# Optimization experiments

Measured on AMD Instinct MI355X. Metric: run time of the kernel, lower is better.

## Reference

```python
import jax, jax.numpy as jnp
import numpy as np

V, E, H, B, TS, TT = 32000, 256, 512, 32, 512, 128


def setup_inputs() -> dict:
    key = jax.random.key(0)
    ks = jax.random.split(key, 20)
    s_e = 1.0 / np.sqrt(E)
    s_h = 1.0 / np.sqrt(H)
    n = jax.random.normal
    return {
        "src": jax.random.randint(ks[0], (B, TS), 0, V),
        "tgt": jax.random.randint(ks[1], (B, TT), 0, V),
        "tf_mask": jax.random.randint(ks[2], (TT - 1,), 0, 2),
        "emb_enc": n(ks[3], (V, E), jnp.float32) * 0.02,
        "emb_dec": n(ks[4], (V, E), jnp.float32) * 0.02,
        "enc_Wih0": n(ks[5], (E, H), jnp.float32) * s_e,
        "enc_Whh0": n(ks[6], (H, H), jnp.float32) * s_h,
        "enc_b0": jnp.zeros((H,), jnp.float32),
        "enc_Wih1": n(ks[7], (H, H), jnp.float32) * s_h,
        "enc_Whh1": n(ks[8], (H, H), jnp.float32) * s_h,
        "enc_b1": jnp.zeros((H,), jnp.float32),
        "dec_Wih0": n(ks[9], (E, H), jnp.float32) * s_e,
        "dec_Whh0": n(ks[10], (H, H), jnp.float32) * s_h,
        "dec_b0": jnp.zeros((H,), jnp.float32),
        "dec_Wih1": n(ks[11], (H, H), jnp.float32) * s_h,
        "dec_Whh1": n(ks[12], (H, H), jnp.float32) * s_h,
        "dec_b1": jnp.zeros((H,), jnp.float32),
        "dec_Wout": n(ks[13], (H, V), jnp.float32) * s_h,
        "dec_bout": jnp.zeros((V,), jnp.float32),
    }


def _cell(x, h, Wih0, Whh0, b0, Wih1, Whh1, b1):
    # x: (B, in), h: (2, B, H) -> new h (2, B, H). Vanilla tanh RNN, 2 layers.
    h0 = jnp.tanh(x @ Wih0 + h[0] @ Whh0 + b0)
    h1 = jnp.tanh(h0 @ Wih1 + h[1] @ Whh1 + b1)
    return jnp.stack([h0, h1])


def reference(src, tgt, tf_mask, emb_enc, emb_dec,
              enc_Wih0, enc_Whh0, enc_b0, enc_Wih1, enc_Whh1, enc_b1,
              dec_Wih0, dec_Whh0, dec_b0, dec_Wih1, dec_Whh1, dec_b1,
              dec_Wout, dec_bout):
    # ---- Encoder: run over TS steps, keep only final hidden (outputs unused by Seq2Seq) ----
    emb = emb_enc[src]                      # (B, TS, E)
    xs = jnp.swapaxes(emb, 0, 1)            # (TS, B, E)
    h0 = jnp.zeros((2, B, H), emb.dtype)

    def enc_step(h, x):
        return _cell(x, h, enc_Wih0, enc_Whh0, enc_b0, enc_Wih1, enc_Whh1, enc_b1), None

    enc_hidden, _ = jax.lax.scan(enc_step, h0, xs)

    def dec_step(carry, inp):
        h, tok = carry
        tgt_t, tf = inp
        x = emb_dec[tok]                    # (B, E)
        h_new = _cell(x, h, dec_Wih0, dec_Whh0, dec_b0, dec_Wih1, dec_Whh1, dec_b1)
        logits = h_new[1] @ dec_Wout + dec_bout   # (B, V)
        greedy = jnp.argmax(logits, axis=1).astype(tok.dtype)
        next_tok = jnp.where(tf > 0, tgt_t, greedy)
        return (h_new, next_tok), logits

    tgt_steps = jnp.swapaxes(tgt[:, 1:], 0, 1)   # (TT-1, B)
    (_, _), logits_seq = jax.lax.scan(dec_step, (enc_hidden, tgt[:, 0]), (tgt_steps, tf_mask))
    return jnp.swapaxes(logits_seq, 0, 1)        # (B, TT-1, V)
```

## Files before the change

kernel.cpp:

```cpp
#include <hip/hip_runtime.h>

#define V  32000
#define E  256
#define H  512
#define BB 32
#define TS 512
#define TT 128
#define NT 127

#define OFF_WBF  0ull
#define OFF_WT   8192000ull
#define OFF_PT   24576000ull
#define OFF_H0   24608000ull
#define OFF_H1   24640768ull
#define OFF_TOK  24673536ull
#define OFF_CNT  24673568ull

__device__ inline unsigned short f2bf(float f){
  unsigned int x = __float_as_uint(f);
  unsigned int r = x + 0x7fffu + ((x >> 16) & 1u);
  return (unsigned short)(r >> 16);
}
__device__ inline float bf2f(unsigned short u){
  return __uint_as_float(((unsigned int)u) << 16);
}

__device__ inline void top2_merge(float& v1,int& i1,float& v2,int& i2,
                                  float o1,int oi1,float o2,int oi2){
  if (o1 > v1 || (o1 == v1 && oi1 < i1)) {
    float nv2; int ni2;
    if (v1 > o2 || (v1 == o2 && i1 < oi2)) { nv2 = v1; ni2 = i1; }
    else { nv2 = o2; ni2 = oi2; }
    v1 = o1; i1 = oi1; v2 = nv2; i2 = ni2;
  } else if (o1 > v2 || (o1 == v2 && oi1 < i2)) {
    v2 = o1; i2 = oi1;
  }
}

__global__ void k_init(float* ws, const int* tgt){
  int gid = blockIdx.x*256 + threadIdx.x;
  float* h0 = ws + OFF_H0; float* h1 = ws + OFF_H1;
  if (gid < 2*BB*H){ h0[gid] = 0.f; h1[gid] = 0.f; }
  if (gid < BB) ((int*)(ws+OFF_TOK))[gid] = tgt[gid*TT + 0];
  if (gid == 0) ((int*)(ws+OFF_CNT))[0] = 0;
}

__global__ void k_wprep(float* ws, const float* wout){
  int tw = blockIdx.x; int k0 = (tw / 500) * 64; int v0 = (tw % 500) * 64;
  __shared__ float tile[64][65];
  unsigned short* wbf = (unsigned short*)(ws + OFF_WBF);
  float* wt = ws + OFF_WT;
  for (int i = threadIdx.x; i < 64*64; i += 256){
    int kk = i >> 6, vv = i & 63;
    float val = wout[(size_t)(k0+kk)*V + v0 + vv];
    tile[kk][vv] = val;
    wbf[(size_t)(k0+kk)*V + v0 + vv] = f2bf(val);
  }
  __syncthreads();
  for (int i = threadIdx.x; i < 64*64; i += 256){
    int vv = i >> 6, kk = i & 63;
    wt[(size_t)(v0+vv)*H + k0 + kk] = tile[kk][vv];
  }
}

__global__ void k_pre0(float* pre0, const int* src, const float* emb,
                       const float* Wih0, const float* b0){
  int t = blockIdx.x >> 2; int cb = blockIdx.x & 3;
  __shared__ int sidx[32];
  __shared__ float sA[32][257];
  int tid = threadIdx.x;
  if (tid < 32) sidx[tid] = src[tid*TS + t];
  __syncthreads();
  for (int i = tid; i < 32*E; i += 256){
    int bb = i >> 8, e = i & 255;
    sA[bb][e] = emb[(size_t)sidx[bb]*E + e];
  }
  __syncthreads();
  int c = tid & 127, rh = tid >> 7;
  int j = cb*128 + c;
  float bj = b0[j];
  float acc[16];
  #pragma unroll
  for (int i=0;i<16;i++) acc[i] = bj;
  for (int k=0;k<E;k++){
    float w = Wih0[(size_t)k*H + j];
    #pragma unroll
    for (int i=0;i<16;i++) acc[i] += sA[rh*16+i][k]*w;
  }
  #pragma unroll
  for (int i=0;i<16;i++){
    int b = rh*16 + i;
    pre0[((size_t)t*BB + b)*H + j] = acc[i];
  }
}

__global__ void k_enc(float* ws, const float* pre0, const float* Whh0,
                      const float* Wih1, const float* Whh1, const float* b1, int tau){
  float* h0 = ws + OFF_H0; float* h1 = ws + OFF_H1;
  int wg = blockIdx.x; int tid = threadIdx.x;
  if (wg < 64){
    if (tau >= TS) return;
    int rb = wg >> 3, cb = wg & 7;
    __shared__ float sh[4][513];
    const float* hprev = h0 + ((tau+1)&1)*BB*H;
    for (int i=tid;i<4*H;i+=256){ int rr=i>>9, k=i&511; sh[rr][k]=hprev[(rb*4+rr)*H+k]; }
    __syncthreads();
    int c = tid & 63, rsub = tid >> 6;
    int r = rb*4 + rsub, j = cb*64 + c;
    const float* w = Whh0 + j;
    float a0=0,a1=0,a2=0,a3=0;
    for (int k=0;k<H;k+=4){
      a0 += sh[rsub][k+0]*w[(size_t)(k+0)*H];
      a1 += sh[rsub][k+1]*w[(size_t)(k+1)*H];
      a2 += sh[rsub][k+2]*w[(size_t)(k+2)*H];
      a3 += sh[rsub][k+3]*w[(size_t)(k+3)*H];
    }
    float acc = pre0[((size_t)tau*BB + r)*H + j] + ((a0+a1)+(a2+a3));
    h0[(tau&1)*BB*H + r*H + j] = tanhf(acc);
  } else {
    if (tau < 1) return;
    int w2 = wg - 64;
    int rb = w2 >> 4, cb = w2 & 15;
    __shared__ float s0[4][513];
    __shared__ float s1[4][513];
    __shared__ float sp[256];
    const float* h0t = h0 + ((tau+1)&1)*BB*H;
    const float* h1p = h1 + (tau&1)*BB*H;
    for (int i=tid;i<4*H;i+=256){
      int rr=i>>9, k=i&511;
      s0[rr][k] = h0t[(rb*4+rr)*H+k];
      s1[rr][k] = h1p[(rb*4+rr)*H+k];
    }
    __syncthreads();
    int kh = tid >> 7, q = tid & 127;
    int c = q & 31, rsub = q >> 5;
    int r = rb*4 + rsub, j = cb*32 + c;
    const float* W = kh ? (Whh1 + j) : (Wih1 + j);
    float (*sh)[513] = kh ? s1 : s0;
    float a0=0,a1=0,a2=0,a3=0;
    for (int k=0;k<H;k+=4){
      a0 += sh[rsub][k+0]*W[(size_t)(k+0)*H];
      a1 += sh[rsub][k+1]*W[(size_t)(k+1)*H];
      a2 += sh[rsub][k+2]*W[(size_t)(k+2)*H];
      a3 += sh[rsub][k+3]*W[(size_t)(k+3)*H];
    }
    sp[tid] = ((a0+a1)+(a2+a3));
    __syncthreads();
    if (kh == 0){
      float v = sp[q] + sp[128+q] + b1[j];
      h1[((tau+1)&1)*BB*H + r*H + j] = tanhf(v);
    }
  }
}

__global__ void k_cellA(float* ws, const float* embd, const float* Wih0,
                        const float* Whh0, const float* b0, int t){
  float* h0 = ws + OFF_H0;
  const int* tok = (const int*)(ws + OFF_TOK);
  int rb = blockIdx.x >> 3, cb = blockIdx.x & 7;
  __shared__ int stok[4];
  __shared__ float sx[4][257];
  __shared__ float sh[4][513];
  int tid = threadIdx.x;
  if (tid < 4) stok[tid] = tok[rb*4 + tid];
  __syncthreads();
  for (int i=tid;i<4*E;i+=256){ int rr=i>>8, e=i&255; sx[rr][e] = embd[(size_t)stok[rr]*E + e]; }
  const float* hprev = h0 + ((t+1)&1)*BB*H;
  for (int i=tid;i<4*H;i+=256){ int rr=i>>9, k=i&511; sh[rr][k] = hprev[(rb*4+rr)*H + k]; }
  __syncthreads();
  int c = tid & 63, rsub = tid >> 6;
  int r = rb*4 + rsub, j = cb*64 + c;
  float a0=0,a1=0,a2=0,a3=0;
  for (int k=0;k<E;k+=4){
    a0 += sx[rsub][k+0]*Wih0[(size_t)(k+0)*H + j];
    a1 += sx[rsub][k+1]*Wih0[(size_t)(k+1)*H + j];
    a2 += sx[rsub][k+2]*Wih0[(size_t)(k+2)*H + j];
    a3 += sx[rsub][k+3]*Wih0[(size_t)(k+3)*H + j];
  }
  for (int k=0;k<H;k+=4){
    a0 += sh[rsub][k+0]*Whh0[(size_t)(k+0)*H + j];
    a1 += sh[rsub][k+1]*Whh0[(size_t)(k+1)*H + j];
    a2 += sh[rsub][k+2]*Whh0[(size_t)(k+2)*H + j];
    a3 += sh[rsub][k+3]*Whh0[(size_t)(k+3)*H + j];
  }
  h0[(t&1)*BB*H + r*H + j] = tanhf(b0[j] + ((a0+a1)+(a2+a3)));
}

__global__ void k_cellB(float* ws, const float* Wih1, const float* Whh1,
                        const float* b1, int t){
  float* h0 = ws + OFF_H0; float* h1 = ws + OFF_H1;
  int rb = blockIdx.x >> 4, cb = blockIdx.x & 15;
  __shared__ float s0[4][513];
  __shared__ float s1[4][513];
  __shared__ float sp[256];
  int tid = threadIdx.x;
  const float* h0c = h0 + (t&1)*BB*H;
  const float* h1p = h1 + ((t+1)&1)*BB*H;
  for (int i=tid;i<4*H;i+=256){
    int rr=i>>9, k=i&511;
    s0[rr][k] = h0c[(rb*4+rr)*H+k];
    s1[rr][k] = h1p[(rb*4+rr)*H+k];
  }
  __syncthreads();
  int kh = tid >> 7, q = tid & 127;
  int c = q & 31, rsub = q >> 5;
  int r = rb*4 + rsub, j = cb*32 + c;
  const float* W = kh ? (Whh1 + j) : (Wih1 + j);
  float (*sh)[513] = kh ? s1 : s0;
  float a0=0,a1=0,a2=0,a3=0;
  for (int k=0;k<H;k+=4){
    a0 += sh[rsub][k+0]*W[(size_t)(k+0)*H];
    a1 += sh[rsub][k+1]*W[(size_t)(k+1)*H];
    a2 += sh[rsub][k+2]*W[(size_t)(k+2)*H];
    a3 += sh[rsub][k+3]*W[(size_t)(k+3)*H];
  }
  sp[tid] = ((a0+a1)+(a2+a3));
  __syncthreads();
  if (kh == 0){
    float v = sp[q] + sp[128+q] + b1[j];
    h1[(t&1)*BB*H + r*H + j] = tanhf(v);
  }
}

__global__ void k_logits(float* ws, float* out, const float* bout,
                         const int* tgt, const int* tf, int t){
  float* h1 = ws + OFF_H1;
  const unsigned short* wbf = (const unsigned short*)(ws + OFF_WBF);
  const float* wt = ws + OFF_WT;
  float* pt = ws + OFF_PT;
  int* tok = (int*)(ws + OFF_TOK);
  int* cnt = (int*)(ws + OFF_CNT);
  int wg = blockIdx.x; int tid = threadIdx.x;
  int rb = wg / 250, cb = wg % 250;
  __shared__ float Lh[16][513];
  const float* h1c = h1 + (t&1)*BB*H;
  for (int i=tid;i<16*H;i+=256){ int rr=i>>9, k=i&511; Lh[rr][k] = h1c[(rb*16+rr)*H + k]; }
  __syncthreads();
  int c = tid & 127, rh = tid >> 7;
  int j = cb*128 + c;
  float bj = bout[j];
  float acc[8];
  #pragma unroll
  for (int i=0;i<8;i++) acc[i] = bj;
  for (int k=0;k<H;k++){
    float w = bf2f(wbf[(size_t)k*V + j]);
    #pragma unroll
    for (int i=0;i<8;i++) acc[i] += Lh[rh*8+i][k]*w;
  }
  #pragma unroll
  for (int i=0;i<8;i++){
    int b = rb*16 + rh*8 + i;
    out[((size_t)b*NT + t)*V + j] = acc[i];
  }
  __shared__ float sv[16][129];
  __shared__ int   si_[16][129];
  #pragma unroll
  for (int i=0;i<8;i++){ sv[rh*8+i][c] = acc[i]; si_[rh*8+i][c] = j; }
  __syncthreads();
  int row = tid >> 4, l16 = tid & 15;
  float v1=-1e30f, v2=-1e30f; int i1=-1, i2=-1;
  for (int s=0;s<8;s++){
    float v = sv[row][l16 + 16*s]; int ix = si_[row][l16 + 16*s];
    top2_merge(v1,i1,v2,i2, v,ix,-1e30f,-1);
  }
  for (int off=8; off>=1; off>>=1){
    float o1 = __shfl_xor(v1, off, 16); int oi1 = __shfl_xor(i1, off, 16);
    float o2 = __shfl_xor(v2, off, 16); int oi2 = __shfl_xor(i2, off, 16);
    top2_merge(v1,i1,v2,i2, o1,oi1,o2,oi2);
  }
  if (l16 == 0){
    int b = rb*16 + row;
    size_t base = ((size_t)cb*32 + b)*4;
    pt[base+0] = v1; ((int*)pt)[base+1] = i1;
    pt[base+2] = v2; ((int*)pt)[base+3] = i2;
  }
  __threadfence();
  __syncthreads();
  __shared__ int lastflag;
  if (tid == 0){
    int old = atomicAdd(cnt, 1);
    lastflag = (old == (int)gridDim.x - 1);
  }
  __syncthreads();
  if (!lastflag) return;
  __threadfence();
  int b = tid >> 3, l = tid & 7;
  float gm = -1e30f;
  for (int cc=l; cc<250; cc+=8) gm = fmaxf(gm, pt[((size_t)cc*32 + b)*4]);
  for (int off=4; off>=1; off>>=1) gm = fmaxf(gm, __shfl_xor(gm, off, 8));
  __shared__ int candn[32];
  __shared__ int candj[32][6];
  if (l == 0) candn[b] = 0;
  __syncthreads();
  float thr = gm - 0.02f;
  for (int cc=l; cc<250; cc+=8){
    #pragma unroll
    for (int s=0;s<2;s++){
      size_t base = ((size_t)cc*32 + b)*4 + s*2;
      float v = pt[base];
      if (v >= thr){
        int slot = atomicAdd(&candn[b], 1);
        if (slot < 6) candj[b][slot] = ((int*)pt)[base+1];
      }
    }
  }
  __syncthreads();
  int n = candn[b]; if (n > 6) n = 6;
  int besti;
  if (n == 1){
    besti = candj[b][0];
  } else {
    float bestv = -1e30f; besti = 0x7fffffff;
    for (int s=0;s<n;s++){
      int jj = candj[b][s];
      const float* wr = wt + (size_t)jj*H;
      const float* hr = h1c + b*H;
      float p = 0.f;
      for (int kk=l*64; kk<l*64+64; kk++) p += hr[kk]*wr[kk];
      for (int off=4; off>=1; off>>=1) p += __shfl_xor(p, off, 8);
      p += bout[jj];
      if (p > bestv || (p == bestv && jj < besti)){ bestv = p; besti = jj; }
    }
  }
  if (l == 0) tok[b] = (tf[t] > 0) ? tgt[b*TT + t + 1] : besti;
  if (tid == 0) *cnt = 0;
}

extern "C" void kernel_launch(void* const* d_in, const int* in_sizes, int n_in,
                              void* d_out, int out_size, void* d_ws, size_t ws_size,
                              hipStream_t stream) {
  (void)in_sizes; (void)n_in; (void)out_size; (void)ws_size;
  const int*   src     = (const int*)  d_in[0];
  const int*   tgt     = (const int*)  d_in[1];
  const int*   tf      = (const int*)  d_in[2];
  const float* emb_enc = (const float*)d_in[3];
  const float* emb_dec = (const float*)d_in[4];
  const float* eW0     = (const float*)d_in[5];
  const float* eU0     = (const float*)d_in[6];
  const float* eb0     = (const float*)d_in[7];
  const float* eW1     = (const float*)d_in[8];
  const float* eU1     = (const float*)d_in[9];
  const float* eb1     = (const float*)d_in[10];
  const float* dW0     = (const float*)d_in[11];
  const float* dU0     = (const float*)d_in[12];
  const float* db0     = (const float*)d_in[13];
  const float* dW1     = (const float*)d_in[14];
  const float* dU1     = (const float*)d_in[15];
  const float* db1     = (const float*)d_in[16];
  const float* Wout    = (const float*)d_in[17];
  const float* bout    = (const float*)d_in[18];
  float* out = (float*)d_out;
  float* ws  = (float*)d_ws;
  float* pre0 = out;

  k_init <<<128, 256, 0, stream>>>(ws, tgt);
  k_wprep<<<4000,256, 0, stream>>>(ws, Wout);
  k_pre0 <<<2048,256, 0, stream>>>(pre0, src, emb_enc, eW0, eb0);
  for (int tau = 0; tau <= TS; ++tau)
    k_enc<<<192, 256, 0, stream>>>(ws, pre0, eU0, eW1, eU1, eb1, tau);
  for (int t = 0; t < NT; ++t){
    k_cellA <<<64,  256, 0, stream>>>(ws, emb_dec, dW0, dU0, db0, t);
    k_cellB <<<128, 256, 0, stream>>>(ws, dW1, dU1, db1, t);
    k_logits<<<500, 256, 0, stream>>>(ws, out, bout, tgt, tf, t);
  }
}
```

Measured before the change: 25.20 ms.

## Replace per-step kernel launches with persistent kernels using grid barriers

The encoder's 513 launches and the decoder's 381 launches are replaced by two persistent kernels. Each step is separated by a software grid barrier built on striped atomic counters, which removes launch overhead and inter-kernel gaps. The bf16 output-projection weights are also stored transposed so each thread can read a contiguous row with 16-byte vector loads. The persistent design relies on all 500 decoder blocks being co-resident, and may deadlock if the hardware cannot schedule them all at once.

```diff
diff --git a/kernel.cpp b/kernel.cpp
--- a/kernel.cpp
+++ b/kernel.cpp
@@ -16,6 +16,10 @@
 #define OFF_TOK  24673536ull
 #define OFF_CNT  24673568ull
 
+typedef unsigned short us8 __attribute__((ext_vector_type(8)));
+
+__device__ int g_bar[256];
+
 __device__ inline unsigned short f2bf(float f){
   unsigned int x = __float_as_uint(f);
   unsigned int r = x + 0x7fffu + ((x >> 16) & 1u);
@@ -23,6 +27,25 @@
 }
 __device__ inline float bf2f(unsigned short u){
   return __uint_as_float(((unsigned int)u) << 16);
+}
+
+#define BARSTRIDE 16
+__device__ __forceinline__ void gridbar(int* base, int target){
+  __syncthreads();
+  if (threadIdx.x == 0){
+    __threadfence();
+    atomicAdd(base + (blockIdx.x & 7)*BARSTRIDE, 1);
+    for (;;){
+      int s = 0;
+      #pragma unroll
+      for (int q = 0; q < 8; q++)
+        s += __hip_atomic_load(base + q*BARSTRIDE, __ATOMIC_RELAXED, __HIP_MEMORY_SCOPE_AGENT);
+      if (s >= target) break;
+      __builtin_amdgcn_s_sleep(2);
+    }
+    __threadfence();
+  }
+  __syncthreads();
 }
 
 __device__ inline void top2_merge(float& v1,int& i1,float& v2,int& i2,
@@ -43,23 +66,24 @@
   if (gid < 2*BB*H){ h0[gid] = 0.f; h1[gid] = 0.f; }
   if (gid < BB) ((int*)(ws+OFF_TOK))[gid] = tgt[gid*TT + 0];
   if (gid == 0) ((int*)(ws+OFF_CNT))[0] = 0;
+  if (gid < 256) g_bar[gid] = 0;
 }
 
 __global__ void k_wprep(float* ws, const float* wout){
   int tw = blockIdx.x; int k0 = (tw / 500) * 64; int v0 = (tw % 500) * 64;
   __shared__ float tile[64][65];
-  unsigned short* wbf = (unsigned short*)(ws + OFF_WBF);
+  unsigned short* wbfT = (unsigned short*)(ws + OFF_WBF);
   float* wt = ws + OFF_WT;
   for (int i = threadIdx.x; i < 64*64; i += 256){
     int kk = i >> 6, vv = i & 63;
-    float val = wout[(size_t)(k0+kk)*V + v0 + vv];
-    tile[kk][vv] = val;
-    wbf[(size_t)(k0+kk)*V + v0 + vv] = f2bf(val);
+    tile[kk][vv] = wout[(size_t)(k0+kk)*V + v0 + vv];
   }
   __syncthreads();
   for (int i = threadIdx.x; i < 64*64; i += 256){
     int vv = i >> 6, kk = i & 63;
-    wt[(size_t)(v0+vv)*H + k0 + kk] = tile[kk][vv];
+    float val = tile[kk][vv];
+    wt  [(size_t)(v0+vv)*H + k0 + kk] = val;
+    wbfT[(size_t)(v0+vv)*H + k0 + kk] = f2bf(val);
   }
 }
 
@@ -94,236 +118,273 @@
   }
 }
 
-__global__ void k_enc(float* ws, const float* pre0, const float* Whh0,
-                      const float* Wih1, const float* Whh1, const float* b1, int tau){
+__global__ __launch_bounds__(256,1) void k_encp(
+    float* __restrict__ ws, const float* __restrict__ pre0,
+    const float* __restrict__ Whh0,
+    const float* __restrict__ Wih1, const float* __restrict__ Whh1,
+    const float* __restrict__ b1)
+{
   float* h0 = ws + OFF_H0; float* h1 = ws + OFF_H1;
-  int wg = blockIdx.x; int tid = threadIdx.x;
-  if (wg < 64){
-    if (tau >= TS) return;
-    int rb = wg >> 3, cb = wg & 7;
-    __shared__ float sh[4][513];
-    const float* hprev = h0 + ((tau+1)&1)*BB*H;
-    for (int i=tid;i<4*H;i+=256){ int rr=i>>9, k=i&511; sh[rr][k]=hprev[(rb*4+rr)*H+k]; }
-    __syncthreads();
-    int c = tid & 63, rsub = tid >> 6;
-    int r = rb*4 + rsub, j = cb*64 + c;
-    const float* w = Whh0 + j;
-    float a0=0,a1=0,a2=0,a3=0;
-    for (int k=0;k<H;k+=4){
-      a0 += sh[rsub][k+0]*w[(size_t)(k+0)*H];
-      a1 += sh[rsub][k+1]*w[(size_t)(k+1)*H];
-      a2 += sh[rsub][k+2]*w[(size_t)(k+2)*H];
-      a3 += sh[rsub][k+3]*w[(size_t)(k+3)*H];
+  const int wg = blockIdx.x; const int tid = threadIdx.x;
+  __shared__ float sh[4*513];
+  __shared__ float s0[4*513];
+  __shared__ float s1[4*513];
+  __shared__ float sp[256];
+  int ep = 0;
+  for (int tau = 0; tau <= TS; ++tau){
+    if (wg < 64){
+      if (tau < TS){
+        int rb = wg >> 3, cb = wg & 7;
+        const float* hprev = h0 + ((tau+1)&1)*BB*H;
+        for (int i=tid;i<4*H;i+=256){ int rr=i>>9, k=i&511; sh[rr*513+k]=hprev[(rb*4+rr)*H+k]; }
+        __syncthreads();
+        int c = tid & 63, rsub = tid >> 6;
+        int r = rb*4 + rsub, j = cb*64 + c;
+        const float* w = Whh0 + j;
+        float a0=0,a1=0,a2=0,a3=0;
+        for (int k=0;k<H;k+=4){
+          a0 += sh[rsub*513+k+0]*w[(size_t)(k+0)*H];
+          a1 += sh[rsub*513+k+1]*w[(size_t)(k+1)*H];
+          a2 += sh[rsub*513+k+2]*w[(size_t)(k+2)*H];
+          a3 += sh[rsub*513+k+3]*w[(size_t)(k+3)*H];
+        }
+        float acc = pre0[((size_t)tau*BB + r)*H + j] + ((a0+a1)+(a2+a3));
+        h0[(tau&1)*BB*H + r*H + j] = tanhf(acc);
+      }
+    } else {
+      if (tau >= 1){
+        int w2 = wg - 64;
+        int rb = w2 >> 4, cb = w2 & 15;
+        const float* h0t = h0 + ((tau+1)&1)*BB*H;
+        const float* h1p = h1 + (tau&1)*BB*H;
+        for (int i=tid;i<4*H;i+=256){
+          int rr=i>>9, k=i&511;
+          s0[rr*513+k] = h0t[(rb*4+rr)*H+k];
+          s1[rr*513+k] = h1p[(rb*4+rr)*H+k];
+        }
+        __syncthreads();
+        int kh = tid >> 7, q = tid & 127;
+        int c = q & 31, rsub = q >> 5;
+        int r = rb*4 + rsub, j = cb*32 + c;
+        const float* W = kh ? (Whh1 + j) : (Wih1 + j);
+        const float* shp = kh ? s1 : s0;
+        float a0=0,a1=0,a2=0,a3=0;
+        for (int k=0;k<H;k+=4){
+          a0 += shp[rsub*513+k+0]*W[(size_t)(k+0)*H];
+          a1 += shp[rsub*513+k+1]*W[(size_t)(k+1)*H];
+          a2 += shp[rsub*513+k+2]*W[(size_t)(k+2)*H];
+          a3 += shp[rsub*513+k+3]*W[(size_t)(k+3)*H];
+        }
+        sp[tid] = ((a0+a1)+(a2+a3));
+        __syncthreads();
+        if (kh == 0){
+          float v = sp[q] + sp[128+q] + b1[j];
+          h1[((tau+1)&1)*BB*H + r*H + j] = tanhf(v);
+        }
+      }
     }
-    float acc = pre0[((size_t)tau*BB + r)*H + j] + ((a0+a1)+(a2+a3));
-    h0[(tau&1)*BB*H + r*H + j] = tanhf(acc);
-  } else {
-    if (tau < 1) return;
-    int w2 = wg - 64;
-    int rb = w2 >> 4, cb = w2 & 15;
-    __shared__ float s0[4][513];
-    __shared__ float s1[4][513];
-    __shared__ float sp[256];
-    const float* h0t = h0 + ((tau+1)&1)*BB*H;
-    const float* h1p = h1 + (tau&1)*BB*H;
-    for (int i=tid;i<4*H;i+=256){
-      int rr=i>>9, k=i&511;
-      s0[rr][k] = h0t[(rb*4+rr)*H+k];
-      s1[rr][k] = h1p[(rb*4+rr)*H+k];
-    }
-    __syncthreads();
-    int kh = tid >> 7, q = tid & 127;
-    int c = q & 31, rsub = q >> 5;
-    int r = rb*4 + rsub, j = cb*32 + c;
-    const float* W = kh ? (Whh1 + j) : (Wih1 + j);
-    float (*sh)[513] = kh ? s1 : s0;
-    float a0=0,a1=0,a2=0,a3=0;
-    for (int k=0;k<H;k+=4){
-      a0 += sh[rsub][k+0]*W[(size_t)(k+0)*H];
-      a1 += sh[rsub][k+1]*W[(size_t)(k+1)*H];
-      a2 += sh[rsub][k+2]*W[(size_t)(k+2)*H];
-      a3 += sh[rsub][k+3]*W[(size_t)(k+3)*H];
-    }
-    sp[tid] = ((a0+a1)+(a2+a3));
-    __syncthreads();
-    if (kh == 0){
-      float v = sp[q] + sp[128+q] + b1[j];
-      h1[((tau+1)&1)*BB*H + r*H + j] = tanhf(v);
-    }
-  }
-}
-
-__global__ void k_cellA(float* ws, const float* embd, const float* Wih0,
-                        const float* Whh0, const float* b0, int t){
-  float* h0 = ws + OFF_H0;
-  const int* tok = (const int*)(ws + OFF_TOK);
-  int rb = blockIdx.x >> 3, cb = blockIdx.x & 7;
-  __shared__ int stok[4];
-  __shared__ float sx[4][257];
-  __shared__ float sh[4][513];
-  int tid = threadIdx.x;
-  if (tid < 4) stok[tid] = tok[rb*4 + tid];
-  __syncthreads();
-  for (int i=tid;i<4*E;i+=256){ int rr=i>>8, e=i&255; sx[rr][e] = embd[(size_t)stok[rr]*E + e]; }
-  const float* hprev = h0 + ((t+1)&1)*BB*H;
-  for (int i=tid;i<4*H;i+=256){ int rr=i>>9, k=i&511; sh[rr][k] = hprev[(rb*4+rr)*H + k]; }
-  __syncthreads();
-  int c = tid & 63, rsub = tid >> 6;
-  int r = rb*4 + rsub, j = cb*64 + c;
-  float a0=0,a1=0,a2=0,a3=0;
-  for (int k=0;k<E;k+=4){
-    a0 += sx[rsub][k+0]*Wih0[(size_t)(k+0)*H + j];
-    a1 += sx[rsub][k+1]*Wih0[(size_t)(k+1)*H + j];
-    a2 += sx[rsub][k+2]*Wih0[(size_t)(k+2)*H + j];
-    a3 += sx[rsub][k+3]*Wih0[(size_t)(k+3)*H + j];
-  }
-  for (int k=0;k<H;k+=4){
-    a0 += sh[rsub][k+0]*Whh0[(size_t)(k+0)*H + j];
-    a1 += sh[rsub][k+1]*Whh0[(size_t)(k+1)*H + j];
-    a2 += sh[rsub][k+2]*Whh0[(size_t)(k+2)*H + j];
-    a3 += sh[rsub][k+3]*Whh0[(size_t)(k+3)*H + j];
-  }
-  h0[(t&1)*BB*H + r*H + j] = tanhf(b0[j] + ((a0+a1)+(a2+a3)));
-}
-
-__global__ void k_cellB(float* ws, const float* Wih1, const float* Whh1,
-                        const float* b1, int t){
+    if (tau < TS){ ++ep; gridbar(g_bar, ep*192); }
+  }
+}
+
+__global__ __launch_bounds__(256,2) void k_decp(
+    float* __restrict__ ws, float* __restrict__ out,
+    const float* __restrict__ embd,
+    const float* __restrict__ Wih0, const float* __restrict__ Whh0, const float* __restrict__ b0,
+    const float* __restrict__ Wih1, const float* __restrict__ Whh1, const float* __restrict__ b1,
+    const float* __restrict__ bout, const int* __restrict__ tgt, const int* __restrict__ tf)
+{
   float* h0 = ws + OFF_H0; float* h1 = ws + OFF_H1;
-  int rb = blockIdx.x >> 4, cb = blockIdx.x & 15;
-  __shared__ float s0[4][513];
-  __shared__ float s1[4][513];
-  __shared__ float sp[256];
-  int tid = threadIdx.x;
-  const float* h0c = h0 + (t&1)*BB*H;
-  const float* h1p = h1 + ((t+1)&1)*BB*H;
-  for (int i=tid;i<4*H;i+=256){
-    int rr=i>>9, k=i&511;
-    s0[rr][k] = h0c[(rb*4+rr)*H+k];
-    s1[rr][k] = h1p[(rb*4+rr)*H+k];
-  }
-  __syncthreads();
-  int kh = tid >> 7, q = tid & 127;
-  int c = q & 31, rsub = q >> 5;
-  int r = rb*4 + rsub, j = cb*32 + c;
-  const float* W = kh ? (Whh1 + j) : (Wih1 + j);
-  float (*sh)[513] = kh ? s1 : s0;
-  float a0=0,a1=0,a2=0,a3=0;
-  for (int k=0;k<H;k+=4){
-    a0 += sh[rsub][k+0]*W[(size_t)(k+0)*H];
-    a1 += sh[rsub][k+1]*W[(size_t)(k+1)*H];
-    a2 += sh[rsub][k+2]*W[(size_t)(k+2)*H];
-    a3 += sh[rsub][k+3]*W[(size_t)(k+3)*H];
-  }
-  sp[tid] = ((a0+a1)+(a2+a3));
-  __syncthreads();
-  if (kh == 0){
-    float v = sp[q] + sp[128+q] + b1[j];
-    h1[(t&1)*BB*H + r*H + j] = tanhf(v);
-  }
-}
-
-__global__ void k_logits(float* ws, float* out, const float* bout,
-                         const int* tgt, const int* tf, int t){
-  float* h1 = ws + OFF_H1;
-  const unsigned short* wbf = (const unsigned short*)(ws + OFF_WBF);
+  const unsigned short* wbfT = (const unsigned short*)(ws + OFF_WBF);
   const float* wt = ws + OFF_WT;
   float* pt = ws + OFF_PT;
   int* tok = (int*)(ws + OFF_TOK);
   int* cnt = (int*)(ws + OFF_CNT);
-  int wg = blockIdx.x; int tid = threadIdx.x;
-  int rb = wg / 250, cb = wg % 250;
-  __shared__ float Lh[16][513];
-  const float* h1c = h1 + (t&1)*BB*H;
-  for (int i=tid;i<16*H;i+=256){ int rr=i>>9, k=i&511; Lh[rr][k] = h1c[(rb*16+rr)*H + k]; }
-  __syncthreads();
-  int c = tid & 127, rh = tid >> 7;
-  int j = cb*128 + c;
-  float bj = bout[j];
-  float acc[8];
-  #pragma unroll
-  for (int i=0;i<8;i++) acc[i] = bj;
-  for (int k=0;k<H;k++){
-    float w = bf2f(wbf[(size_t)k*V + j]);
-    #pragma unroll
-    for (int i=0;i<8;i++) acc[i] += Lh[rh*8+i][k]*w;
-  }
-  #pragma unroll
-  for (int i=0;i<8;i++){
-    int b = rb*16 + rh*8 + i;
-    out[((size_t)b*NT + t)*V + j] = acc[i];
-  }
-  __shared__ float sv[16][129];
-  __shared__ int   si_[16][129];
-  #pragma unroll
-  for (int i=0;i<8;i++){ sv[rh*8+i][c] = acc[i]; si_[rh*8+i][c] = j; }
-  __syncthreads();
-  int row = tid >> 4, l16 = tid & 15;
-  float v1=-1e30f, v2=-1e30f; int i1=-1, i2=-1;
-  for (int s=0;s<8;s++){
-    float v = sv[row][l16 + 16*s]; int ix = si_[row][l16 + 16*s];
-    top2_merge(v1,i1,v2,i2, v,ix,-1e30f,-1);
-  }
-  for (int off=8; off>=1; off>>=1){
-    float o1 = __shfl_xor(v1, off, 16); int oi1 = __shfl_xor(i1, off, 16);
-    float o2 = __shfl_xor(v2, off, 16); int oi2 = __shfl_xor(i2, off, 16);
-    top2_merge(v1,i1,v2,i2, o1,oi1,o2,oi2);
-  }
-  if (l16 == 0){
-    int b = rb*16 + row;
-    size_t base = ((size_t)cb*32 + b)*4;
-    pt[base+0] = v1; ((int*)pt)[base+1] = i1;
-    pt[base+2] = v2; ((int*)pt)[base+3] = i2;
-  }
-  __threadfence();
-  __syncthreads();
+  const int blk = blockIdx.x; const int tid = threadIdx.x;
+  int* bar = g_bar + 128;
+
+  __shared__ __align__(16) float smem[12384];
   __shared__ int lastflag;
-  if (tid == 0){
-    int old = atomicAdd(cnt, 1);
-    lastflag = (old == (int)gridDim.x - 1);
-  }
-  __syncthreads();
-  if (!lastflag) return;
-  __threadfence();
-  int b = tid >> 3, l = tid & 7;
-  float gm = -1e30f;
-  for (int cc=l; cc<250; cc+=8) gm = fmaxf(gm, pt[((size_t)cc*32 + b)*4]);
-  for (int off=4; off>=1; off>>=1) gm = fmaxf(gm, __shfl_xor(gm, off, 8));
   __shared__ int candn[32];
   __shared__ int candj[32][6];
-  if (l == 0) candn[b] = 0;
-  __syncthreads();
-  float thr = gm - 0.02f;
-  for (int cc=l; cc<250; cc+=8){
-    #pragma unroll
-    for (int s=0;s<2;s++){
-      size_t base = ((size_t)cc*32 + b)*4 + s*2;
-      float v = pt[base];
-      if (v >= thr){
-        int slot = atomicAdd(&candn[b], 1);
-        if (slot < 6) candj[b][slot] = ((int*)pt)[base+1];
-      }
+
+  int ep = 0;
+  for (int t = 0; t < NT; ++t){
+    if (blk < 64){
+      int rb = blk >> 3, cb = blk & 7;
+      int*   stok = (int*)smem;
+      float* sx   = smem + 4;
+      float* shh  = smem + 4 + 4*257;
+      if (tid < 4) stok[tid] = tok[rb*4 + tid];
+      __syncthreads();
+      for (int i=tid;i<4*E;i+=256){ int rr=i>>8, e=i&255; sx[rr*257+e] = embd[(size_t)stok[rr]*E + e]; }
+      const float* hprev = h0 + ((t+1)&1)*BB*H;
+      for (int i=tid;i<4*H;i+=256){ int rr=i>>9, k=i&511; shh[rr*513+k] = hprev[(rb*4+rr)*H + k]; }
+      __syncthreads();
+      int c = tid & 63, rsub = tid >> 6;
+      int r = rb*4 + rsub, j = cb*64 + c;
+      float a0=0,a1=0,a2=0,a3=0;
+      for (int k=0;k<E;k+=4){
+        a0 += sx[rsub*257+k+0]*Wih0[(size_t)(k+0)*H + j];
+        a1 += sx[rsub*257+k+1]*Wih0[(size_t)(k+1)*H + j];
+        a2 += sx[rsub*257+k+2]*Wih0[(size_t)(k+2)*H + j];
+        a3 += sx[rsub*257+k+3]*Wih0[(size_t)(k+3)*H + j];
+      }
+      for (int k=0;k<H;k+=4){
+        a0 += shh[rsub*513+k+0]*Whh0[(size_t)(k+0)*H + j];
+        a1 += shh[rsub*513+k+1]*Whh0[(size_t)(k+1)*H + j];
+        a2 += shh[rsub*513+k+2]*Whh0[(size_t)(k+2)*H + j];
+        a3 += shh[rsub*513+k+3]*Whh0[(size_t)(k+3)*H + j];
+      }
+      h0[(t&1)*BB*H + r*H + j] = tanhf(b0[j] + ((a0+a1)+(a2+a3)));
     }
-  }
-  __syncthreads();
-  int n = candn[b]; if (n > 6) n = 6;
-  int besti;
-  if (n == 1){
-    besti = candj[b][0];
-  } else {
-    float bestv = -1e30f; besti = 0x7fffffff;
-    for (int s=0;s<n;s++){
-      int jj = candj[b][s];
-      const float* wr = wt + (size_t)jj*H;
-      const float* hr = h1c + b*H;
-      float p = 0.f;
-      for (int kk=l*64; kk<l*64+64; kk++) p += hr[kk]*wr[kk];
-      for (int off=4; off>=1; off>>=1) p += __shfl_xor(p, off, 8);
-      p += bout[jj];
-      if (p > bestv || (p == bestv && jj < besti)){ bestv = p; besti = jj; }
+    ++ep; gridbar(bar, ep*500);
+
+    if (blk < 128){
+      int rb = blk >> 4, cb = blk & 15;
+      float* s0 = smem;
+      float* s1 = smem + 2052;
+      float* sp = smem + 4104;
+      const float* h0c = h0 + (t&1)*BB*H;
+      const float* h1p = h1 + ((t+1)&1)*BB*H;
+      for (int i=tid;i<4*H;i+=256){
+        int rr=i>>9, k=i&511;
+        s0[rr*513+k] = h0c[(rb*4+rr)*H+k];
+        s1[rr*513+k] = h1p[(rb*4+rr)*H+k];
+      }
+      __syncthreads();
+      int kh = tid >> 7, q = tid & 127;
+      int c = q & 31, rsub = q >> 5;
+      int r = rb*4 + rsub, j = cb*32 + c;
+      const float* W = kh ? (Whh1 + j) : (Wih1 + j);
+      const float* shp = kh ? s1 : s0;
+      float a0=0,a1=0,a2=0,a3=0;
+      for (int k=0;k<H;k+=4){
+        a0 += shp[rsub*513+k+0]*W[(size_t)(k+0)*H];
+        a1 += shp[rsub*513+k+1]*W[(size_t)(k+1)*H];
+        a2 += shp[rsub*513+k+2]*W[(size_t)(k+2)*H];
+        a3 += shp[rsub*513+k+3]*W[(size_t)(k+3)*H];
+      }
+      sp[tid] = ((a0+a1)+(a2+a3));
+      __syncthreads();
+      if (kh == 0){
+        float v = sp[q] + sp[128+q] + b1[j];
+        h1[(t&1)*BB*H + r*H + j] = tanhf(v);
+      }
     }
-  }
-  if (l == 0) tok[b] = (tf[t] > 0) ? tgt[b*TT + t + 1] : besti;
-  if (tid == 0) *cnt = 0;
+    ++ep; gridbar(bar, ep*500);
+
+    {
+      int rb = blk / 250, cb = blk % 250;
+      float* Lh  = smem;
+      float* sv  = smem + 16*516;
+      int*   si_ = (int*)(smem + 16*516 + 16*129);
+      const float* h1c = h1 + (t&1)*BB*H;
+      for (int i=tid;i<16*H;i+=256){ int rr=i>>9, k=i&511; Lh[rr*516+k] = h1c[(rb*16+rr)*H + k]; }
+      __syncthreads();
+      int c = tid & 127, rh = tid >> 7;
+      int j = cb*128 + c;
+      float bj = bout[j];
+      float acc[8];
+      #pragma unroll
+      for (int i=0;i<8;i++) acc[i] = bj;
+      const unsigned short* wr = wbfT + (size_t)j*H;
+      for (int k=0;k<H;k+=16){
+        us8 wa = *(const us8*)(wr + k);
+        us8 wb = *(const us8*)(wr + k + 8);
+        float wf[16];
+        #pragma unroll
+        for (int q=0;q<8;q++) wf[q]   = bf2f(wa[q]);
+        #pragma unroll
+        for (int q=0;q<8;q++) wf[8+q] = bf2f(wb[q]);
+        #pragma unroll
+        for (int i=0;i<8;i++){
+          const float4* hp = (const float4*)(Lh + (rh*8+i)*516 + k);
+          float4 hA = hp[0], hB = hp[1], hC = hp[2], hD = hp[3];
+          float s = acc[i];
+          s += hA.x*wf[0];  s += hA.y*wf[1];  s += hA.z*wf[2];  s += hA.w*wf[3];
+          s += hB.x*wf[4];  s += hB.y*wf[5];  s += hB.z*wf[6];  s += hB.w*wf[7];
+          s += hC.x*wf[8];  s += hC.y*wf[9];  s += hC.z*wf[10]; s += hC.w*wf[11];
+          s += hD.x*wf[12]; s += hD.y*wf[13]; s += hD.z*wf[14]; s += hD.w*wf[15];
+          acc[i] = s;
+        }
+      }
+      #pragma unroll
+      for (int i=0;i<8;i++){
+        int b = rb*16 + rh*8 + i;
+        out[((size_t)b*NT + t)*V + j] = acc[i];
+      }
+      #pragma unroll
+      for (int i=0;i<8;i++){ sv[(rh*8+i)*129 + c] = acc[i]; si_[(rh*8+i)*129 + c] = j; }
+      __syncthreads();
+      int row = tid >> 4, l16 = tid & 15;
+      float v1=-1e30f, v2=-1e30f; int i1=-1, i2=-1;
+      for (int s=0;s<8;s++){
+        float v = sv[row*129 + l16 + 16*s]; int ix = si_[row*129 + l16 + 16*s];
+        top2_merge(v1,i1,v2,i2, v,ix,-1e30f,-1);
+      }
+      for (int off=8; off>=1; off>>=1){
+        float o1 = __shfl_xor(v1, off, 16); int oi1 = __shfl_xor(i1, off, 16);
+        float o2 = __shfl_xor(v2, off, 16); int oi2 = __shfl_xor(i2, off, 16);
+        top2_merge(v1,i1,v2,i2, o1,oi1,o2,oi2);
+      }
+      if (l16 == 0){
+        int b = rb*16 + row;
+        size_t base = ((size_t)cb*32 + b)*4;
+        pt[base+0] = v1; ((int*)pt)[base+1] = i1;
+        pt[base+2] = v2; ((int*)pt)[base+3] = i2;
+      }
+      __threadfence();
+      __syncthreads();
+      if (tid == 0){
+        int old = atomicAdd(cnt, 1);
+        lastflag = (old == 499);
+      }
+      __syncthreads();
+      if (lastflag){
+        __threadfence();
+        int b = tid >> 3, l = tid & 7;
+        float gm = -1e30f;
+        for (int cc=l; cc<250; cc+=8) gm = fmaxf(gm, pt[((size_t)cc*32 + b)*4]);
+        for (int off=4; off>=1; off>>=1) gm = fmaxf(gm, __shfl_xor(gm, off, 8));
+        if (l == 0) candn[b] = 0;
+        __syncthreads();
+        float thr = gm - 0.02f;
+        for (int cc=l; cc<250; cc+=8){
+          #pragma unroll
+          for (int s=0;s<2;s++){
+            size_t base = ((size_t)cc*32 + b)*4 + s*2;
+            float v = pt[base];
+            if (v >= thr){
+              int slot = atomicAdd(&candn[b], 1);
+              if (slot < 6) candj[b][slot] = ((int*)pt)[base+1];
+            }
+          }
+        }
+        __syncthreads();
+        int n = candn[b]; if (n > 6) n = 6;
+        int besti;
+        if (n == 1){
+          besti = candj[b][0];
+        } else {
+          float bestv = -1e30f; besti = 0x7fffffff;
+          for (int s=0;s<n;s++){
+            int jj = candj[b][s];
+            const float* wrow = wt + (size_t)jj*H;
+            const float* hr = h1c + b*H;
+            float p = 0.f;
+            for (int kk=l*64; kk<l*64+64; kk++) p += hr[kk]*wrow[kk];
+            for (int off=4; off>=1; off>>=1) p += __shfl_xor(p, off, 8);
+            p += bout[jj];
+            if (p > bestv || (p == bestv && jj < besti)){ bestv = p; besti = jj; }
+          }
+        }
+        if (l == 0) tok[b] = (tf[t] > 0) ? tgt[b*TT + t + 1] : besti;
+        if (tid == 0) *cnt = 0;
+      }
+    }
+    ++ep; gridbar(bar, ep*500);
+  }
 }
 
 extern "C" void kernel_launch(void* const* d_in, const int* in_sizes, int n_in,
@@ -356,11 +417,7 @@
   k_init <<<128, 256, 0, stream>>>(ws, tgt);
   k_wprep<<<4000,256, 0, stream>>>(ws, Wout);
   k_pre0 <<<2048,256, 0, stream>>>(pre0, src, emb_enc, eW0, eb0);
-  for (int tau = 0; tau <= TS; ++tau)
-    k_enc<<<192, 256, 0, stream>>>(ws, pre0, eU0, eW1, eU1, eb1, tau);
-  for (int t = 0; t < NT; ++t){
-    k_cellA <<<64,  256, 0, stream>>>(ws, emb_dec, dW0, dU0, db0, t);
-    k_cellB <<<128, 256, 0, stream>>>(ws, dW1, dU1, db1, t);
-    k_logits<<<500, 256, 0, stream>>>(ws, out, bout, tgt, tf, t);
-  }
-}
+  k_encp <<<192, 256, 0, stream>>>(ws, pre0, eU0, eW1, eU1, eb1);
+  k_decp <<<500, 256, 0, stream>>>(ws, out, emb_dec, dW0, dU0, db0,
+                                   dW1, dU1, db1, bout, tgt, tf);
+}
```

After: 58.42 ms. +131.8%, slower.
